# Kernel tuning notes

Hardware: AMD Instinct MI355X
Metric: run time of the kernel (lower is better)

## Reference

```python
import jax, jax.numpy as jnp
import numpy as np

B, S, D = 2, 2048, 1024
H = 16
K = 21  # tisa_num_kernels
HD = D // H


def setup_inputs() -> dict:
    key = jax.random.key(0)
    ks = jax.random.split(key, 7)
    x = jax.random.normal(ks[0], (B, S, D), dtype=jnp.float32)
    # in_proj: Linear(d_model, 3*d_model, bias=False); stored as (D, 3D) for x @ w
    w_in = jax.random.normal(ks[1], (D, 3 * D), dtype=jnp.float32) * (1.0 / np.sqrt(D))
    # gate: Linear(d_model, 2*d_model) with bias
    w_gate = jax.random.normal(ks[2], (D, 2 * D), dtype=jnp.float32) * (1.0 / np.sqrt(D))
    b_gate = jnp.zeros((2 * D,), dtype=jnp.float32)
    # TISA kernel params, one set of K kernels per head
    amplitudes = jax.random.normal(ks[3], (H, K), dtype=jnp.float32) * 0.1
    sharpness = jax.random.uniform(ks[4], (H, K), dtype=jnp.float32, minval=0.05, maxval=0.3)
    max_fv, min_fv = S // 2, 5
    offsets = jax.random.uniform(ks[5], (H, K), dtype=jnp.float32, minval=-float(max_fv), maxval=float(max_fv))
    return {"x": x, "w_in": w_in, "w_gate": w_gate, "b_gate": b_gate,
            "amplitudes": amplitudes, "sharpness": sharpness, "offsets": offsets}


def _tisa_bias(amplitudes, sharpness, offsets, seq_len):
    # Translation-invariant: score depends only on relative position j - i.
    # Compute scores over the 2S-1 unique relative positions, then gather.
    rel = jnp.arange(-(seq_len - 1), seq_len, dtype=jnp.float32)  # (2S-1,)
    # (H, K, 2S-1)
    d = rel[None, None, :] - offsets[:, :, None]
    scores = amplitudes[:, :, None] * jnp.exp(-jnp.abs(sharpness)[:, :, None] * d * d)
    scores = scores.sum(axis=1)  # (H, 2S-1)
    idx = jnp.arange(seq_len)
    rel_idx = idx[None, :] - idx[:, None] + (seq_len - 1)  # (S, S) in [0, 2S-2]
    return scores[:, rel_idx]  # (H, S, S)


def reference(x, w_in, w_gate, b_gate, amplitudes, sharpness, offsets):
    b, s, d = x.shape
    proj = x @ w_in  # (B, S, 3D); layout: [k | v | q]
    k, v, q = jnp.split(proj, 3, axis=-1)

    def heads(t):  # (B, S, D) -> (B, H, S, HD)
        return t.reshape(b, s, H, HD).transpose(0, 2, 1, 3)

    q, k, v = heads(q), heads(k), heads(v)
    scale = 1.0 / jnp.sqrt(jnp.float32(HD))
    scores = jnp.einsum('bhqd,bhkd->bhqk', q, k) * scale  # (B, H, S, S)
    scores = scores + _tisa_bias(amplitudes, sharpness, offsets, s)[None]
    weights = jax.nn.softmax(scores, axis=-1)
    attn = jnp.einsum('bhqk,bhkd->bhqd', weights, v)  # (B, H, S, HD)
    out = attn.transpose(0, 2, 1, 3).reshape(b, s, d)  # (B, S, D)
    gated = out @ w_gate + b_gate  # (B, S, 2D)
    a, g = jnp.split(gated, 2, axis=-1)
    return a * jax.nn.sigmoid(g)
```

## Files before the change

### kernel.cpp

```cpp
#include <hip/hip_runtime.h>
#include <math.h>

#define B_   2
#define S_   2048
#define D_   1024
#define H_   16
#define K_   21
#define HD_  64
#define D3_  3072
#define D2_  2048
#define REL_ 4095

typedef __attribute__((ext_vector_type(8))) short bf16x8;
typedef __attribute__((ext_vector_type(8))) unsigned short u16x8;
typedef __attribute__((ext_vector_type(4))) float f32x4;

#define MFMA16(a, b, c) __builtin_amdgcn_mfma_f32_16x16x32_bf16((a), (b), (c), 0, 0, 0)

__device__ __forceinline__ unsigned short f2bf(float f) {
    union { float f; unsigned u; } v; v.f = f;
    return (unsigned short)((v.u + 0x7fffu + ((v.u >> 16) & 1u)) >> 16);
}
__device__ __forceinline__ float bf2f(unsigned short h) {
    union { unsigned u; float f; } v; v.u = ((unsigned)h) << 16;
    return v.f;
}
__device__ __forceinline__ float asf(unsigned u) {
    union { unsigned u; float f; } v; v.u = u; return v.f;
}
__device__ __forceinline__ unsigned cvtpk(float a, float b) {
    unsigned r;
    asm("v_cvt_pk_bf16_f32 %0, %1, %2" : "=v"(r) : "v"(a), "v"(b));
    return r;
}
#define SPLIT8(f, ph, pl)                                                      \
    {                                                                          \
        _Pragma("unroll")                                                      \
        for (int _t = 0; _t < 4; ++_t) ph.u[_t] = cvtpk(f[2*_t], f[2*_t+1]);   \
        _Pragma("unroll")                                                      \
        for (int _t = 0; _t < 4; ++_t) {                                       \
            float _h0 = asf(ph.u[_t] << 16);                                   \
            float _h1 = asf(ph.u[_t] & 0xffff0000u);                           \
            pl.u[_t] = cvtpk(f[2*_t] - _h0, f[2*_t+1] - _h1);                  \
        }                                                                      \
    }

__device__ __forceinline__ void gload16(const void* g, void* l) {
    __builtin_amdgcn_global_load_lds(
        (const __attribute__((address_space(1))) unsigned int*)g,
        (__attribute__((address_space(3))) unsigned int*)l, 16, 0, 0);
}

__global__ void tisa_bias_kernel(const float* __restrict__ amp,
                                 const float* __restrict__ shp,
                                 const float* __restrict__ off,
                                 float* __restrict__ bias_rel) {
    int idx = blockIdx.x * blockDim.x + threadIdx.x;
    if (idx >= H_ * REL_) return;
    int h = idx / REL_;
    int r = idx - h * REL_;
    float rel = (float)(r - (S_ - 1));
    float acc = 0.f;
    #pragma unroll
    for (int k = 0; k < K_; ++k) {
        float d = rel - off[h * K_ + k];
        acc = fmaf(amp[h * K_ + k], expf(-fabsf(shp[h * K_ + k]) * d * d), acc);
    }
    bias_rel[idx] = acc;
}

template<bool PERM>
__global__ __launch_bounds__(256) void convert_wT_kernel(
    const float* __restrict__ in, unsigned short* __restrict__ out, int Kd, int N)
{
    __shared__ float t[64][65];
    const int tid = threadIdx.x;
    const int k0 = blockIdx.y * 64;
    const int n0 = blockIdx.x * 64;
    {
        const int r  = tid >> 2;
        const int cq = (tid & 3) * 16;
        #pragma unroll
        for (int e = 0; e < 4; ++e) {
            float4 v = *(const float4*)&in[(size_t)(k0 + r) * N + n0 + cq + 4 * e];
            t[r][cq + 4 * e + 0] = v.x;
            t[r][cq + 4 * e + 1] = v.y;
            t[r][cq + 4 * e + 2] = v.z;
            t[r][cq + 4 * e + 3] = v.w;
        }
    }
    __syncthreads();
    {
        const int n  = tid >> 2;
        const int ks = (tid & 3) * 16;
        const int nkc = Kd >> 5;
        unsigned short hi[16], lo[16];
        #pragma unroll
        for (int i = 0; i < 16; ++i) {
            float v = t[ks + i][n];
            hi[i] = f2bf(v);
            lo[i] = f2bf(v - bf2f(hi[i]));
        }
        const int kg = k0 + ks;
        const int kc = kg >> 5;
        const int j0 = kg & 31;
        const int nsrc = n0 + n;
        const int dc = PERM ? ((nsrc < 1024) ? 2 * nsrc : 2 * (nsrc - 1024) + 1) : nsrc;
        unsigned short* op = out + (size_t)dc * (nkc * 64) + kc * 64;
        *(u16x8*)&op[j0]          = *(u16x8*)&hi[0];
        *(u16x8*)&op[j0 + 8]      = *(u16x8*)&hi[8];
        *(u16x8*)&op[32 + j0]     = *(u16x8*)&lo[0];
        *(u16x8*)&op[32 + j0 + 8] = *(u16x8*)&lo[8];
    }
}

template<bool ASPLIT, int EPI>
__global__ __launch_bounds__(256) void gemm_split_kernel(
    const void* Ap, const unsigned short* __restrict__ Bt,
    const float* __restrict__ bias, float* C,
    int N, int Kd, int lda, int ldc)
{
    __shared__ unsigned short Al[128 * 64];
    __shared__ unsigned short Bl[128 * 64];
    const int tid  = threadIdx.x;
    const int w    = tid >> 6;
    const int lane = tid & 63;
    const int c    = lane & 15;
    const int g    = lane >> 4;
    const int m0   = blockIdx.y * 128;
    const int n0   = blockIdx.x * 128;
    const int wrow = (w >> 1) * 64;
    const int wcol = (w & 1) * 64;
    const int nkc  = Kd >> 5;

    f32x4 acc[4][4];
    #pragma unroll
    for (int i = 0; i < 4; ++i)
        #pragma unroll
        for (int j = 0; j < 4; ++j) acc[i][j] = (f32x4){0.f, 0.f, 0.f, 0.f};

    const int srowB  = w * 8 + (lane >> 3);
    const int sslotB = lane & 7;

    for (int kc = 0; kc < nkc; ++kc) {
        if (ASPLIT) {
            #pragma unroll
            for (int i = 0; i < 4; ++i) {
                const int row = w * 32 + i * 8 + (lane >> 3);
                const char* src = (const char*)Ap + (size_t)(m0 + row) * lda
                                + kc * 128 + (((lane & 7) ^ (row & 7)) << 4);
                gload16(src, (char*)Al + w * 4096 + i * 1024);
            }
        } else {
            const int am  = tid >> 1;
            const int ah_ = tid & 1;
            const float* ap = (const float*)Ap + (size_t)(m0 + am) * lda + kc * 32 + ah_ * 16;
            float v[16];
            #pragma unroll
            for (int e = 0; e < 4; ++e)
                *(float4*)&v[4 * e] = *(const float4*)(ap + 4 * e);
            union { unsigned u[4]; bf16x8 v; } h0, l0, h1, l1;
            {
                const float* f = v;     SPLIT8(f, h0, l0);
            }
            {
                const float* f = v + 8; SPLIT8(f, h1, l1);
            }
            char* rowp = (char*)Al + am * 128;
            *(uint4*)(rowp + (((2 * ah_ + 0) ^ (am & 7)) << 4)) = *(uint4*)&h0.u[0];
            *(uint4*)(rowp + (((2 * ah_ + 1) ^ (am & 7)) << 4)) = *(uint4*)&h1.u[0];
            *(uint4*)(rowp + (((4 + 2 * ah_ + 0) ^ (am & 7)) << 4)) = *(uint4*)&l0.u[0];
            *(uint4*)(rowp + (((4 + 2 * ah_ + 1) ^ (am & 7)) << 4)) = *(uint4*)&l1.u[0];
        }
        #pragma unroll
        for (int i = 0; i < 4; ++i) {
            const int n = i * 32 + srowB;
            const unsigned short* src = Bt
                + ((size_t)(n0 + n) * nkc + kc) * 64 + ((sslotB ^ (n & 7)) << 3);
            gload16(src, (char*)Bl + i * 4096 + w * 1024);
        }
        __syncthreads();

        bf16x8 ah[4], al[4], bh[4], bl[4];
        #pragma unroll
        for (int f = 0; f < 4; ++f) {
            const int m = wrow + f * 16 + c;
            const char* rp = (const char*)Al + m * 128;
            ah[f] = *(const bf16x8*)(rp + (((g + 0) ^ (m & 7)) << 4));
            al[f] = *(const bf16x8*)(rp + (((g + 4) ^ (m & 7)) << 4));
            const int n = wcol + f * 16 + c;
            const char* rq = (const char*)Bl + n * 128;
            bh[f] = *(const bf16x8*)(rq + (((g + 0) ^ (n & 7)) << 4));
            bl[f] = *(const bf16x8*)(rq + (((g + 4) ^ (n & 7)) << 4));
        }
        #pragma unroll
        for (int mf = 0; mf < 4; ++mf)
            #pragma unroll
            for (int nf = 0; nf < 4; ++nf) {
                acc[mf][nf] = MFMA16(ah[mf], bh[nf], acc[mf][nf]);
                acc[mf][nf] = MFMA16(al[mf], bh[nf], acc[mf][nf]);
                acc[mf][nf] = MFMA16(ah[mf], bl[nf], acc[mf][nf]);
            }
        __syncthreads();
    }

    if (EPI == 1) {
        if (n0 < 1024) {
            #pragma unroll
            for (int mf = 0; mf < 4; ++mf)
                #pragma unroll
                for (int r = 0; r < 4; ++r) {
                    const int row = m0 + wrow + mf * 16 + g * 4 + r;
                    char* rowB = (char*)C + (size_t)row * 12288;
                    #pragma unroll
                    for (int nf = 0; nf < 4; ++nf) {
                        const int col = n0 + wcol + nf * 16 + c;
                        const float val = acc[mf][nf][r];
                        const unsigned short hi = f2bf(val);
                        *(unsigned short*)(rowB + 4096 + 2 * col) = hi;
                        *(unsigned short*)(rowB + 6144 + 2 * col) = f2bf(val - bf2f(hi));
                    }
                }
        } else if (n0 < 2048) {
            #pragma unroll
            for (int mf = 0; mf < 4; ++mf) {
                const int row0 = m0 + wrow + mf * 16 + g * 4;
                const int s2 = (row0 & 2047) * 2;
                const size_t ibase = (size_t)(row0 >> 11) * 1024;
                #pragma unroll
                for (int nf = 0; nf < 4; ++nf) {
                    const int d = n0 - 1024 + wcol + nf * 16 + c;
                    ushort4 hv, lv;
                    {
                        float v0 = acc[mf][nf][0], v1 = acc[mf][nf][1];
                        float v2 = acc[mf][nf][2], v3 = acc[mf][nf][3];
                        hv.x = f2bf(v0); lv.x = f2bf(v0 - bf2f(hv.x));
                        hv.y = f2bf(v1); lv.y = f2bf(v1 - bf2f(hv.y));
                        hv.z = f2bf(v2); lv.z = f2bf(v2 - bf2f(hv.z));
                        hv.w = f2bf(v3); lv.w = f2bf(v3 - bf2f(hv.w));
                    }
                    char* base = (char*)C + (ibase + d) * (size_t)24576 + s2;
                    *(ushort4*)base           = hv;
                    *(ushort4*)(base + 12288) = lv;
                }
            }
        } else {
            #pragma unroll
            for (int mf = 0; mf < 4; ++mf)
                #pragma unroll
                for (int r = 0; r < 4; ++r) {
                    const int row = m0 + wrow + mf * 16 + g * 4 + r;
                    float* cp = &C[(size_t)row * ldc + n0 + wcol + c];
                    #pragma unroll
                    for (int nf = 0; nf < 4; ++nf)
                        cp[nf * 16] = acc[mf][nf][r];
                }
        }
    } else {
        float bgs[4];
        #pragma unroll
        for (int nf = 0; nf < 4; ++nf) {
            const int jc = n0 + wcol + nf * 16 + c;
            bgs[nf] = bias[(jc & 1) ? (1024 + (jc >> 1)) : (jc >> 1)];
        }
        #pragma unroll
        for (int mf = 0; mf < 4; ++mf)
            #pragma unroll
            for (int r = 0; r < 4; ++r) {
                const int row = m0 + wrow + mf * 16 + g * 4 + r;
                #pragma unroll
                for (int nf = 0; nf < 4; ++nf) {
                    const int jc = n0 + wcol + nf * 16 + c;
                    const float val = acc[mf][nf][r] + bgs[nf];
                    const float part = __shfl_xor(val, 1);
                    if (!(c & 1))
                        C[(size_t)row * ldc + (jc >> 1)] = val / (1.f + __expf(-part));
                }
            }
    }
}

__global__ __launch_bounds__(256) void attn_mfma_kernel(
    const float* projf, char* projB, const float* __restrict__ bias_rel)
{
    __shared__ unsigned short KHI[4096], KLO[4096], VHI[4096], VLO[4096];
    __shared__ unsigned P32[4096];
    __shared__ float bias_s[128];

    const int tid  = threadIdx.x;
    const int w    = tid >> 6;
    const int lane = tid & 63;
    const int c    = lane & 15;
    const int g    = lane >> 4;
    const int h    = blockIdx.y;
    const int b    = blockIdx.z;
    const int qbase = blockIdx.x * 64;
    const size_t rowbase = (size_t)b * S_;

    bf16x8 Qhi[2], Qlo[2];
    {
        const float* qp = projf + (rowbase + qbase + 16 * w + c) * D3_ + 2 * D_ + h * HD_;
        #pragma unroll
        for (int ck = 0; ck < 2; ++ck) {
            float q8[8];
            *(float4*)&q8[0] = *(const float4*)(qp + ck * 32 + g * 8);
            *(float4*)&q8[4] = *(const float4*)(qp + ck * 32 + g * 8 + 4);
            union { unsigned u[4]; bf16x8 v; } ph, pl;
            const float* f = q8;
            SPLIT8(f, ph, pl);
            Qhi[ck] = ph.v;
            Qlo[ck] = pl.v;
        }
    }

    f32x4 o_acc[4];
    #pragma unroll
    for (int n = 0; n < 4; ++n) o_acc[n] = (f32x4){0.f, 0.f, 0.f, 0.f};
    float m_run = -INFINITY;
    float l_run = 0.f;

    for (int kt = 0; kt < S_ / 64; ++kt) {
        const int kbase = kt * 64;
        __syncthreads();

        #pragma unroll
        for (int i = 0; i < 2; ++i) {
            const int row = w * 16 + i * 8 + (lane >> 3);
            const int gs  = (lane & 7) ^ (row & 7);
            const int dst = (w * 16 + i * 8) * 128;
            const char* ks = projB + (rowbase + kbase + row) * (size_t)12288
                           + 4096 + h * 128 + gs * 16;
            gload16(ks,        (char*)KHI + dst);
            gload16(ks + 2048, (char*)KLO + dst);
            const char* vs = projB + (size_t)(b * 1024 + h * HD_ + row) * 24576
                           + (size_t)kbase * 2 + gs * 16;
            gload16(vs,         (char*)VHI + dst);
            gload16(vs + 12288, (char*)VLO + dst);
        }
        if (tid < 127)
            bias_s[tid] = bias_rel[h * REL_ + kbase - qbase + tid + 1984];
        __syncthreads();

        f32x4 sf[4];
        #pragma unroll
        for (int f = 0; f < 4; ++f) {
            f32x4 acc = (f32x4){0.f, 0.f, 0.f, 0.f};
            const int krow = f * 16 + c;
            const unsigned short* kbp = KHI + krow * 64;
            const unsigned short* klp = KLO + krow * 64;
            #pragma unroll
            for (int ck = 0; ck < 2; ++ck) {
                const int s = ((ck * 4 + g) ^ (krow & 7)) * 8;
                bf16x8 kh  = *(const bf16x8*)(kbp + s);
                bf16x8 kl8 = *(const bf16x8*)(klp + s);
                acc = MFMA16(kh, Qhi[ck], acc);
                acc = MFMA16(kl8, Qhi[ck], acc);
                acc = MFMA16(kh, Qlo[ck], acc);
            }
            sf[f] = acc;
        }

        #pragma unroll
        for (int f = 0; f < 4; ++f) {
            const int tb = 16 * f + 4 * g - 16 * w - c + 63;
            #pragma unroll
            for (int r = 0; r < 4; ++r)
                sf[f][r] = fmaf(sf[f][r], 0.125f, bias_s[tb + r]);
        }

        float pm[4];
        #pragma unroll
        for (int f = 0; f < 4; ++f)
            pm[f] = fmaxf(fmaxf(sf[f][0], sf[f][1]), fmaxf(sf[f][2], sf[f][3]));
        float mt = fmaxf(fmaxf(pm[0], pm[1]), fmaxf(pm[2], pm[3]));
        mt = fmaxf(mt, __shfl_xor(mt, 16));
        mt = fmaxf(mt, __shfl_xor(mt, 32));
        const float mn = fmaxf(m_run, mt);
        const float sc = __expf(m_run - mn);
        float ps[4];
        #pragma unroll
        for (int f = 0; f < 4; ++f) {
            #pragma unroll
            for (int r = 0; r < 4; ++r)
                sf[f][r] = __expf(sf[f][r] - mn);
            ps[f] = (sf[f][0] + sf[f][1]) + (sf[f][2] + sf[f][3]);
        }
        float rs = (ps[0] + ps[1]) + (ps[2] + ps[3]);
        rs += __shfl_xor(rs, 16);
        rs += __shfl_xor(rs, 32);
        l_run = l_run * sc + rs;
        m_run = mn;

        #pragma unroll
        for (int r = 0; r < 4; ++r) {
            const float scr = __shfl(sc, 20 * g + r);
            #pragma unroll
            for (int n = 0; n < 4; ++n) o_acc[n][r] *= scr;
        }

        #pragma unroll
        for (int f = 0; f < 4; ++f)
            *(f32x4*)&P32[(((16 * w + c) * 64 + 16 * f + 4 * g)) ^ ((c & 7) << 2)] = sf[f];
        asm volatile("s_waitcnt lgkmcnt(0)" ::: "memory");

        #pragma unroll
        for (int ck = 0; ck < 2; ++ck) {
            const int base = (16 * w + c) * 64 + ck * 32 + g * 8;
            const int x = (c & 7) << 2;
            uint4 w0 = *(const uint4*)&P32[base ^ x];
            uint4 w1 = *(const uint4*)&P32[(base + 4) ^ x];
            float pf[8] = {asf(w0.x), asf(w0.y), asf(w0.z), asf(w0.w),
                           asf(w1.x), asf(w1.y), asf(w1.z), asf(w1.w)};
            union { unsigned u[4]; bf16x8 v; } ph, pl;
            const float* fp = pf;
            SPLIT8(fp, ph, pl);
            #pragma unroll
            for (int n = 0; n < 4; ++n) {
                const int d = 16 * n + c;
                const int s = ((ck * 4 + g) ^ (d & 7)) * 8;
                bf16x8 vh = *(const bf16x8*)(VHI + d * 64 + s);
                bf16x8 vl = *(const bf16x8*)(VLO + d * 64 + s);
                o_acc[n] = MFMA16(ph.v, vh, o_acc[n]);
                o_acc[n] = MFMA16(pl.v, vh, o_acc[n]);
                o_acc[n] = MFMA16(ph.v, vl, o_acc[n]);
            }
        }
    }

    const float inv = 1.f / l_run;
    #pragma unroll
    for (int r = 0; r < 4; ++r) {
        const float invr = __shfl(inv, 20 * g + r);
        unsigned short* op = (unsigned short*)(projB
            + (rowbase + qbase + 16 * w + 4 * g + r) * (size_t)12288 + 8192);
        #pragma unroll
        for (int n = 0; n < 4; ++n) {
            const float v = o_acc[n][r] * invr;
            const int col = h * HD_ + 16 * n + c;
            const int kc2 = col >> 5;
            const int j   = col & 31;
            const unsigned short hi = f2bf(v);
            op[kc2 * 64 + j]      = hi;
            op[kc2 * 64 + 32 + j] = f2bf(v - bf2f(hi));
        }
    }
}

extern "C" void kernel_launch(void* const* d_in, const int* in_sizes, int n_in,
                              void* d_out, int out_size, void* d_ws, size_t ws_size,
                              hipStream_t stream) {
    const float* x      = (const float*)d_in[0];
    const float* w_in   = (const float*)d_in[1];
    const float* w_gate = (const float*)d_in[2];
    const float* b_gate = (const float*)d_in[3];
    const float* amp    = (const float*)d_in[4];
    const float* shp    = (const float*)d_in[5];
    const float* off    = (const float*)d_in[6];
    float* outp = (float*)d_out;

    char* ws = (char*)d_ws;
    float*    proj     = (float*)ws;
    float*    bias_rel = (float*)(ws + 50331648);
    unsigned short* wT = (unsigned short*)(ws + 50331648 + 262144);

    tisa_bias_kernel<<<(H_ * REL_ + 255) / 256, 256, 0, stream>>>(amp, shp, off, bias_rel);
    convert_wT_kernel<false><<<dim3(D3_ / 64, D_ / 64), 256, 0, stream>>>(w_in, wT, D_, D3_);
    gemm_split_kernel<false, 1><<<dim3(D3_ / 128, (B_ * S_) / 128), 256, 0, stream>>>(
        x, wT, nullptr, proj, D3_, D_, D_, D3_);
    convert_wT_kernel<true><<<dim3(D2_ / 64, D_ / 64), 256, 0, stream>>>(w_gate, wT, D_, D2_);
    attn_mfma_kernel<<<dim3(S_ / 64, H_, B_), 256, 0, stream>>>(proj, ws, bias_rel);
    gemm_split_kernel<true, 2><<<dim3(D2_ / 128, (B_ * S_) / 128), 256, 0, stream>>>(
        ws + 8192, wT, b_gate, outp, D2_, D_, 12288, D_);
}
```

Measured before the change: 332.8 us.

## Register-prefetch next K/V tile, remap blocks per XCD, lazy softmax rescale

The attention kernel now loads the next K/V and bias tile into registers while the current tile is being computed, then stores it to LDS after the barrier. Before, it used direct global-to-LDS loads that stalled each iteration. The launch grid is flattened to 1D and remapped so that all query tiles of one (head, batch) pair land on the same XCD, which improves L2 reuse of K/V. The online softmax skips rescaling the output accumulator unless the running max grows by more than 8, which removes per-tile multiplies and shuffles. The cost is higher register pressure and a bounded exponent growth that could affect accuracy.

After: 321.6 us. 3.3% less time.

```diff
diff --git a/kernel.cpp b/kernel.cpp
--- a/kernel.cpp
+++ b/kernel.cpp
@@ -292,9 +292,14 @@
     const int lane = tid & 63;
     const int c    = lane & 15;
     const int g    = lane >> 4;
-    const int h    = blockIdx.y;
-    const int b    = blockIdx.z;
-    const int qbase = blockIdx.x * 64;
+    const int bid  = blockIdx.x;
+    const int xcd  = bid & 7;
+    const int slot = bid >> 3;
+    const int qt   = slot & 31;
+    const int p    = (slot >> 5) * 8 + xcd;
+    const int h    = p >> 1;
+    const int b    = p & 1;
+    const int qbase = qt * 64;
     const size_t rowbase = (size_t)b * S_;
 
     bf16x8 Qhi[2], Qlo[2];
@@ -319,26 +324,42 @@
     float m_run = -INFINITY;
     float l_run = 0.f;
 
+    const int srow0 = w * 16 + (lane >> 3);
+    const int gs0   = (lane & 7) ^ (srow0 & 7);
+    uint4 rk0h, rk0l, rk1h, rk1l, rv0h, rv0l, rv1h, rv1l;
+    float breg = 0.f;
+
+#define LOADKV(ktv)                                                            \
+    {                                                                          \
+        const int kbase_ = (ktv) * 64;                                         \
+        const char* ks0 = projB + (rowbase + kbase_ + srow0) * (size_t)12288   \
+                        + 4096 + h * 128 + gs0 * 16;                           \
+        const char* ks1 = ks0 + 8 * 12288;                                     \
+        rk0h = *(const uint4*)ks0;  rk0l = *(const uint4*)(ks0 + 2048);        \
+        rk1h = *(const uint4*)ks1;  rk1l = *(const uint4*)(ks1 + 2048);        \
+        const char* vs0 = projB + (size_t)(b * 1024 + h * HD_ + srow0) * 24576 \
+                        + (size_t)kbase_ * 2 + gs0 * 16;                       \
+        const char* vs1 = vs0 + 8 * 24576;                                     \
+        rv0h = *(const uint4*)vs0;  rv0l = *(const uint4*)(vs0 + 12288);       \
+        rv1h = *(const uint4*)vs1;  rv1l = *(const uint4*)(vs1 + 12288);       \
+        if (tid < 127)                                                         \
+            breg = bias_rel[h * REL_ + kbase_ - qbase + tid + 1984];           \
+    }
+
+    LOADKV(0);
+
     for (int kt = 0; kt < S_ / 64; ++kt) {
-        const int kbase = kt * 64;
         __syncthreads();
-
-        #pragma unroll
-        for (int i = 0; i < 2; ++i) {
-            const int row = w * 16 + i * 8 + (lane >> 3);
-            const int gs  = (lane & 7) ^ (row & 7);
-            const int dst = (w * 16 + i * 8) * 128;
-            const char* ks = projB + (rowbase + kbase + row) * (size_t)12288
-                           + 4096 + h * 128 + gs * 16;
-            gload16(ks,        (char*)KHI + dst);
-            gload16(ks + 2048, (char*)KLO + dst);
-            const char* vs = projB + (size_t)(b * 1024 + h * HD_ + row) * 24576
-                           + (size_t)kbase * 2 + gs * 16;
-            gload16(vs,         (char*)VHI + dst);
-            gload16(vs + 12288, (char*)VLO + dst);
-        }
-        if (tid < 127)
-            bias_s[tid] = bias_rel[h * REL_ + kbase - qbase + tid + 1984];
+        {
+            const int d0 = srow0 * 128 + (lane & 7) * 16;
+            const int d1 = d0 + 1024;
+            *(uint4*)((char*)KHI + d0) = rk0h; *(uint4*)((char*)KHI + d1) = rk1h;
+            *(uint4*)((char*)KLO + d0) = rk0l; *(uint4*)((char*)KLO + d1) = rk1l;
+            *(uint4*)((char*)VHI + d0) = rv0h; *(uint4*)((char*)VHI + d1) = rv1h;
+            *(uint4*)((char*)VLO + d0) = rv0l; *(uint4*)((char*)VLO + d1) = rv1l;
+            if (tid < 127) bias_s[tid] = breg;
+        }
+        if (kt + 1 < S_ / 64) LOADKV(kt + 1);
         __syncthreads();
 
         f32x4 sf[4];
@@ -375,28 +396,30 @@
         float mt = fmaxf(fmaxf(pm[0], pm[1]), fmaxf(pm[2], pm[3]));
         mt = fmaxf(mt, __shfl_xor(mt, 16));
         mt = fmaxf(mt, __shfl_xor(mt, 32));
-        const float mn = fmaxf(m_run, mt);
-        const float sc = __expf(m_run - mn);
+        if (!__all(mt <= m_run + 8.f)) {
+            const float mn = fmaxf(m_run, mt);
+            const float sc = __expf(m_run - mn);
+            l_run *= sc;
+            m_run = mn;
+            #pragma unroll
+            for (int r = 0; r < 4; ++r) {
+                const float scr = __shfl(sc, 20 * g + r);
+                #pragma unroll
+                for (int n = 0; n < 4; ++n) o_acc[n][r] *= scr;
+            }
+        }
         float ps[4];
         #pragma unroll
         for (int f = 0; f < 4; ++f) {
             #pragma unroll
             for (int r = 0; r < 4; ++r)
-                sf[f][r] = __expf(sf[f][r] - mn);
+                sf[f][r] = __expf(sf[f][r] - m_run);
             ps[f] = (sf[f][0] + sf[f][1]) + (sf[f][2] + sf[f][3]);
         }
         float rs = (ps[0] + ps[1]) + (ps[2] + ps[3]);
         rs += __shfl_xor(rs, 16);
         rs += __shfl_xor(rs, 32);
-        l_run = l_run * sc + rs;
-        m_run = mn;
-
-        #pragma unroll
-        for (int r = 0; r < 4; ++r) {
-            const float scr = __shfl(sc, 20 * g + r);
-            #pragma unroll
-            for (int n = 0; n < 4; ++n) o_acc[n][r] *= scr;
-        }
+        l_run += rs;
 
         #pragma unroll
         for (int f = 0; f < 4; ++f)
@@ -426,6 +449,7 @@
             }
         }
     }
+#undef LOADKV
 
     const float inv = 1.f / l_run;
     #pragma unroll
@@ -468,7 +492,7 @@
     gemm_split_kernel<false, 1><<<dim3(D3_ / 128, (B_ * S_) / 128), 256, 0, stream>>>(
         x, wT, nullptr, proj, D3_, D_, D_, D3_);
     convert_wT_kernel<true><<<dim3(D2_ / 64, D_ / 64), 256, 0, stream>>>(w_gate, wT, D_, D2_);
-    attn_mfma_kernel<<<dim3(S_ / 64, H_, B_), 256, 0, stream>>>(proj, ws, bias_rel);
+    attn_mfma_kernel<<<1024, 256, 0, stream>>>(proj, ws, bias_rel);
     gemm_split_kernel<true, 2><<<dim3(D2_ / 128, (B_ * S_) / 128), 256, 0, stream>>>(
         ws + 8192, wT, b_gate, outp, D2_, D_, 12288, D_);
 }
```
